# Kernel tuning notes

Hardware: AMD Instinct MI355X
Metric: run time of the kernel (lower is better)

Reference implementation:

```python
import jax, jax.numpy as jnp
import numpy as np

B, T, C = 8, 2048, 1024      # batch, timesteps, input_dim
G, E = 2, 320                # groups_dim, entries_dim
EMB = 512                    # emb_dim
D = EMB // G                 # true_emb_dim per group


def setup_inputs() -> dict:
    key = jax.random.key(0)
    k1, k2, k3 = jax.random.split(key, 3)
    X = jax.random.normal(k1, (B, T, C), dtype=jnp.float32)
    # nn.Linear(input_dim, G*E): weight (out,in) ~ N(0,1), bias zeros
    W = jax.random.normal(k2, (G * E, C), dtype=jnp.float32)
    b = jnp.zeros((G * E,), dtype=jnp.float32)
    # codebook Parameter(1, G*E, D) ~ U[0,1); stored squeezed as (G*E, D)
    codebook = jax.random.uniform(k3, (G * E, D), dtype=jnp.float32)
    return {"X": X, "W": W, "b": b, "codebook": codebook}


def reference(X, W, b, codebook):
    # Eval-mode forward of VectorQuantization (time_first=True).
    nB, nT, _ = X.shape
    logits = jnp.einsum("btc,kc->btk", X, W) + b           # (B, T, G*E)
    # Faithful to source: view (B,T,G*E) as (B*G, T*E) and argmax over last dim
    flat = logits.reshape(nB * G, nT * E)                   # (B*G, T*E)
    k = jnp.argmax(flat, axis=-1)                           # (B*G,)
    hard = jax.nn.one_hot(k, nT * E, dtype=logits.dtype)    # (B*G, T*E)
    q = hard.reshape(nB * nT, G, E)                         # (B*T, G, E)
    # (one-hot * codebook).sum over entries == per-group gather
    cb = codebook.reshape(G, E, D)                          # (G, E, D)
    out = jnp.einsum("nge,ged->ngd", q, cb)                 # (B*T, G, D)
    return out.reshape(nB, nT, G * D)                       # (B, T, emb_dim)
```

## Files before the change

kernel.cpp:

```cpp
#include <hip/hip_runtime.h>
#include <stdint.h>

#define CC    1024
#define EE    320
#define KN    640
#define DD    256
#define MTOT  16384
#define NBLK  640
#define OUT4  2097152
#define MARGIN 2.0f

typedef __attribute__((ext_vector_type(8))) short short8;
typedef __attribute__((ext_vector_type(4))) float f32x4;

__device__ __forceinline__ unsigned int f32_orderable(float x) {
    unsigned int b = __float_as_uint(x);
    return (b & 0x80000000u) ? ~b : (b | 0x80000000u);
}

__device__ __forceinline__ unsigned short bf16_rne(float x) {
    unsigned int u = __float_as_uint(x);
    return (unsigned short)((u + 0x7FFFu + ((u >> 16) & 1u)) >> 16);
}

__global__ void init_slots_kernel(unsigned long long* __restrict__ slots) {
    if (threadIdx.x < 17) slots[threadIdx.x] = 0ull;
}

__global__ __launch_bounds__(256)
void convert_kernel(const float* __restrict__ X, const float* __restrict__ W,
                    unsigned short* __restrict__ A2F, unsigned short* __restrict__ B2F,
                    unsigned long long* __restrict__ slots, float* __restrict__ out) {
    const int bid = blockIdx.x;
    const int tid = threadIdx.x;
    {
        int zidx = bid * 256 + tid;
        f32x4 z = {0.f, 0.f, 0.f, 0.f};
        if (zidx < OUT4) __builtin_nontemporal_store(z, (f32x4*)out + zidx);
    }
    const int lane = tid & 63;
    const float* src;
    unsigned short* dst;
    int unit;
    if (bid < 8192) {
        unit = (bid & 7) * 4096 + (bid >> 3) * 4 + (tid >> 6);
        src = X; dst = A2F;
    } else {
        if (bid == 8192 && tid < 17) slots[tid] = 0ull;
        unit = (bid - 8192) * 4 + (tid >> 6);
        src = W; dst = B2F;
    }
    int rt = unit >> 5, kc = unit & 31;
    int row = rt * 16 + (lane & 15);
    int col = kc * 32 + ((lane >> 4) << 3);
    const float* p = src + (size_t)row * CC + col;
    float4 v0 = *(const float4*)p;
    float4 v1 = *(const float4*)(p + 4);
    short8 hi;
    hi[0] = (short)bf16_rne(v0.x); hi[1] = (short)bf16_rne(v0.y);
    hi[2] = (short)bf16_rne(v0.z); hi[3] = (short)bf16_rne(v0.w);
    hi[4] = (short)bf16_rne(v1.x); hi[5] = (short)bf16_rne(v1.y);
    hi[6] = (short)bf16_rne(v1.z); hi[7] = (short)bf16_rne(v1.w);
    __builtin_nontemporal_store(hi, (short8*)(dst + (size_t)unit * 512 + lane * 8));
}

__global__ __launch_bounds__(256, 3)
void gemm_argmax_mfma(const unsigned short* __restrict__ A2F,
                      const unsigned short* __restrict__ B2F,
                      const float* __restrict__ X,
                      const float* __restrict__ W,
                      const float* __restrict__ bias,
                      const float* __restrict__ codebook,
                      float* __restrict__ out,
                      unsigned long long* __restrict__ slots,
                      unsigned int* __restrict__ counter) {
    __shared__ float redf[4];
    __shared__ int cnt_s;
    __shared__ int cand_s[128];
    __shared__ unsigned int done_s;
    __shared__ unsigned long long s16[16];

    const int tid  = threadIdx.x;
    const int lane = tid & 63;
    const int wave = tid >> 6;

    const int l   = blockIdx.x;
    const int xcd = l & 7;
    const int w   = l >> 3;
    const int mt  = xcd * 16 + w / 5;
    const int nt  = w % 5;
    const int m0 = mt * 128;
    const int n0 = nt * 128;

    const int wm = (wave >> 1) * 64;
    const int wn = (wave & 1) * 64;

    const unsigned short* Ap[4];
    const unsigned short* Bp[4];
#pragma unroll
    for (int t = 0; t < 4; t++) {
        Ap[t] = A2F + ((size_t)(((m0 + wm) >> 4) + t) * 32) * 512 + lane * 8;
        Bp[t] = B2F + ((size_t)(((n0 + wn) >> 4) + t) * 32) * 512 + lane * 8;
    }

    f32x4 acc[4][4] = {};
    short8 a0[4], b0[4], a1[4], b1[4];

#pragma unroll
    for (int t = 0; t < 4; t++) {
        a0[t] = *(const short8*)(Ap[t]);
        b0[t] = *(const short8*)(Bp[t]);
        Ap[t] += 512; Bp[t] += 512;
    }

#define STEP(CURA, CURB, NXTA, NXTB, IT)                                         \
    {                                                                            \
        if ((IT) < 31) {                                                         \
            _Pragma("unroll")                                                    \
            for (int t = 0; t < 4; t++) {                                        \
                NXTA[t] = *(const short8*)(Ap[t]);                               \
                NXTB[t] = *(const short8*)(Bp[t]);                               \
                Ap[t] += 512; Bp[t] += 512;                                      \
            }                                                                    \
        }                                                                        \
        _Pragma("unroll")                                                        \
        for (int ti = 0; ti < 4; ti++)                                           \
            _Pragma("unroll")                                                    \
            for (int tj = 0; tj < 4; tj++)                                       \
                acc[ti][tj] = __builtin_amdgcn_mfma_f32_16x16x32_bf16(           \
                    CURA[ti], CURB[tj], acc[ti][tj], 0, 0, 0);                   \
    }

    for (int it2 = 0; it2 < 16; it2++) {
        STEP(a0, b0, a1, b1, it2 * 2)
        STEP(a1, b1, a0, b0, it2 * 2 + 1)
    }
#undef STEP

    float bias4[4];
#pragma unroll
    for (int tj = 0; tj < 4; tj++) bias4[tj] = bias[n0 + wn + tj * 16 + (lane & 15)];

    float vmax = -3.0e38f;
#pragma unroll
    for (int ti = 0; ti < 4; ti++)
#pragma unroll
        for (int tj = 0; tj < 4; tj++)
#pragma unroll
            for (int r = 0; r < 4; r++)
                vmax = fmaxf(vmax, acc[ti][tj][r] + bias4[tj]);
#pragma unroll
    for (int off = 32; off > 0; off >>= 1)
        vmax = fmaxf(vmax, __shfl_down(vmax, off, 64));
    if (lane == 0) redf[wave] = vmax;
    if (tid == 0) cnt_s = 0;
    __syncthreads();
    float bm = fmaxf(fmaxf(redf[0], redf[1]), fmaxf(redf[2], redf[3]));
    float thresh = bm - MARGIN;

#pragma unroll
    for (int ti = 0; ti < 4; ti++) {
#pragma unroll
        for (int r = 0; r < 4; r++) {
            int m = m0 + wm + ti * 16 + (lane >> 4) * 4 + r;
#pragma unroll
            for (int tj = 0; tj < 4; tj++) {
                float v = acc[ti][tj][r] + bias4[tj];
                if (v >= thresh) {
                    int n = n0 + wn + tj * 16 + (lane & 15);
                    int idx = atomicAdd(&cnt_s, 1);
                    if (idx < 128) cand_s[idx] = (m << 10) | n;
                }
            }
        }
    }
    __syncthreads();
    int cnt = cnt_s < 128 ? cnt_s : 128;

    for (int i = 0; i < cnt; i++) {
        int mc = cand_s[i] >> 10;
        int nc = cand_s[i] & 1023;
        float4 xv = *(const float4*)(X + (size_t)mc * CC + tid * 4);
        float4 wv = *(const float4*)(W + (size_t)nc * CC + tid * 4);
        float p = xv.x * wv.x + xv.y * wv.y + xv.z * wv.z + xv.w * wv.w;
#pragma unroll
        for (int off = 32; off > 0; off >>= 1) p += __shfl_down(p, off, 64);
        if (lane == 0) redf[wave] = p;
        __syncthreads();
        if (tid == 0) {
            float tot = redf[0] + redf[1] + redf[2] + redf[3] + bias[nc];
            unsigned int c = (unsigned int)((mc & 1023) * KN + nc);
            unsigned long long pk =
                ((unsigned long long)f32_orderable(tot) << 32) |
                (unsigned long long)(~c);
            atomicMax(slots + (mc >> 10), pk);
        }
        __syncthreads();
    }

    if (tid == 0) {
        __threadfence();
        done_s = atomicAdd(counter, 1u);
    }
    __syncthreads();

    if (done_s == NBLK - 1) {
        if (tid < 16) s16[tid] = atomicAdd(slots + tid, 0ull);
        __syncthreads();
        int rr  = tid >> 4;
        int seg = tid & 15;
        unsigned long long p = s16[rr];
        unsigned int c = ~(unsigned int)(p & 0xFFFFFFFFull);
        int tl = (int)(c / KN);
        int kg = (int)(c % KN);
        int b  = rr >> 1, h = rr & 1;
        int nstar = b * 2048 + h * 1024 + tl;
        int g = kg / EE;
        const float4* src = (const float4*)(codebook + (size_t)kg * DD) + seg * 4;
        float4* dst = (float4*)(out + (size_t)nstar * 512 + (size_t)g * DD) + seg * 4;
#pragma unroll
        for (int j = 0; j < 4; j++) dst[j] = src[j];
    }
}

__global__ __launch_bounds__(256)
void zs_kernel(const unsigned long long* __restrict__ slots,
               const float* __restrict__ codebook,
               float4* __restrict__ out4) {
    int i4 = blockIdx.x * 256 + threadIdx.x;
    int n  = i4 >> 7;
    int c4 = i4 & 127;
    int b  = n >> 11;
    int h  = (n >> 10) & 1;
    unsigned long long p = slots[b * 2 + h];
    unsigned int c = ~(unsigned int)(p & 0xFFFFFFFFull);
    int tl = (int)(c / KN);
    int kg = (int)(c % KN);
    int nstar = b * 2048 + h * 1024 + tl;
    int g = kg / EE;
    float4 v = make_float4(0.f, 0.f, 0.f, 0.f);
    if (n == nstar && (c4 >> 6) == g)
        v = ((const float4*)codebook)[kg * 64 + (c4 & 63)];
    out4[i4] = v;
}

#define BM 128
#define BN 64
#define BK 32
#define LDA (BM + 4)
#define LDB (BN + 4)

__global__ __launch_bounds__(128)
void gemm_argmax_f32(const float* __restrict__ X, const float* __restrict__ W,
                     const float* __restrict__ bias,
                     unsigned long long* __restrict__ slots) {
    __shared__ float Asf[BK][LDA];
    __shared__ float Bsf[BK][LDB];
    const int tid = threadIdx.x;
    const int m0 = blockIdx.y * BM;
    const int n0 = blockIdx.x * BN;
    const int tx = tid & 7, ty = tid >> 3;
    float acc[8][8];
#pragma unroll
    for (int i = 0; i < 8; i++)
#pragma unroll
        for (int j = 0; j < 8; j++) acc[i][j] = 0.0f;
    const int lm = tid >> 3, lk = (tid & 7) * 4;
    const float* Xb = X + (size_t)m0 * CC;
    const float* Wb = W + (size_t)n0 * CC;
    for (int k0 = 0; k0 < CC; k0 += BK) {
#pragma unroll
        for (int r = 0; r < 8; r++) {
            int m = r * 16 + lm;
            float4 v = *(const float4*)(Xb + (size_t)m * CC + k0 + lk);
            Asf[lk + 0][m] = v.x; Asf[lk + 1][m] = v.y; Asf[lk + 2][m] = v.z; Asf[lk + 3][m] = v.w;
        }
#pragma unroll
        for (int r = 0; r < 4; r++) {
            int m = r * 16 + lm;
            float4 v = *(const float4*)(Wb + (size_t)m * CC + k0 + lk);
            Bsf[lk + 0][m] = v.x; Bsf[lk + 1][m] = v.y; Bsf[lk + 2][m] = v.z; Bsf[lk + 3][m] = v.w;
        }
        __syncthreads();
#pragma unroll
        for (int kk = 0; kk < BK; kk++) {
            float4 A0 = *(const float4*)&Asf[kk][ty * 8];
            float4 A1 = *(const float4*)&Asf[kk][ty * 8 + 4];
            float4 B0 = *(const float4*)&Bsf[kk][tx * 8];
            float4 B1 = *(const float4*)&Bsf[kk][tx * 8 + 4];
            float a[8] = {A0.x, A0.y, A0.z, A0.w, A1.x, A1.y, A1.z, A1.w};
            float b[8] = {B0.x, B0.y, B0.z, B0.w, B1.x, B1.y, B1.z, B1.w};
#pragma unroll
            for (int i = 0; i < 8; i++)
#pragma unroll
                for (int j = 0; j < 8; j++) acc[i][j] = fmaf(a[i], b[j], acc[i][j]);
        }
        __syncthreads();
    }
    unsigned long long best = 0ull;
#pragma unroll
    for (int i = 0; i < 8; i++) {
        int mg = m0 + ty * 8 + i;
        int tl = mg & 1023;
#pragma unroll
        for (int j = 0; j < 8; j++) {
            int kg = n0 + tx * 8 + j;
            float v = acc[i][j] + bias[kg];
            unsigned int c = (unsigned int)(tl * KN + kg);
            unsigned long long p = ((unsigned long long)f32_orderable(v) << 32) |
                                   (unsigned long long)(~c);
            if (p > best) best = p;
        }
    }
#pragma unroll
    for (int off = 32; off > 0; off >>= 1) {
        unsigned long long o = __shfl_down(best, off, 64);
        if (o > best) best = o;
    }
    __shared__ unsigned long long red2[2];
    if ((tid & 63) == 0) red2[tid >> 6] = best;
    __syncthreads();
    if (tid == 0) {
        unsigned long long b0 = red2[0], b1 = red2[1];
        atomicMax(slots + (m0 >> 10), b0 > b1 ? b0 : b1);
    }
}

extern "C" void kernel_launch(void* const* d_in, const int* in_sizes, int n_in,
                              void* d_out, int out_size, void* d_ws, size_t ws_size,
                              hipStream_t stream) {
    const float* X        = (const float*)d_in[0];
    const float* W        = (const float*)d_in[1];
    const float* bias     = (const float*)d_in[2];
    const float* codebook = (const float*)d_in[3];
    float* out = (float*)d_out;

    unsigned long long* slots = (unsigned long long*)d_ws;
    unsigned int* counter = (unsigned int*)(slots + 16);
    const size_t A_off   = 256;
    const size_t A_bytes = (size_t)MTOT * CC * 2;
    const size_t B_off   = A_off + A_bytes;
    const size_t B_bytes = (size_t)KN * CC * 2;
    const size_t need = B_off + B_bytes;

    if (ws_size >= need) {
        unsigned short* A2F = (unsigned short*)((char*)d_ws + A_off);
        unsigned short* B2F = (unsigned short*)((char*)d_ws + B_off);
        hipLaunchKernelGGL(convert_kernel, dim3(8192 + 320), dim3(256), 0, stream,
                           X, W, A2F, B2F, slots, out);
        hipLaunchKernelGGL(gemm_argmax_mfma, dim3(NBLK), dim3(256), 0, stream,
                           A2F, B2F, X, W, bias, codebook, out, slots, counter);
    } else {
        hipLaunchKernelGGL(init_slots_kernel, dim3(1), dim3(64), 0, stream, slots);
        hipLaunchKernelGGL(gemm_argmax_f32, dim3(KN / BN, MTOT / BM), dim3(128), 0, stream,
                           X, W, bias, slots);
        hipLaunchKernelGGL(zs_kernel, dim3(OUT4 / 256), dim3(256), 0, stream,
                           slots, codebook, (float4*)out);
    }
}
```

Before: 168.9 us.

## Switch argmax GEMM prefilter from bf16 to fp8 MFMA with wider margin

```diff
diff --git a/kernel.cpp b/kernel.cpp
--- a/kernel.cpp
+++ b/kernel.cpp
@@ -8,65 +8,69 @@
 #define MTOT  16384
 #define NBLK  640
 #define OUT4  2097152
-#define MARGIN 2.0f
+#define MARGIN 12.0f
 
 typedef __attribute__((ext_vector_type(8))) short short8;
 typedef __attribute__((ext_vector_type(4))) float f32x4;
+typedef __attribute__((ext_vector_type(2))) long longx2;
 
 __device__ __forceinline__ unsigned int f32_orderable(float x) {
     unsigned int b = __float_as_uint(x);
     return (b & 0x80000000u) ? ~b : (b | 0x80000000u);
 }
 
-__device__ __forceinline__ unsigned short bf16_rne(float x) {
-    unsigned int u = __float_as_uint(x);
-    return (unsigned short)((u + 0x7FFFu + ((u >> 16) & 1u)) >> 16);
-}
-
 __global__ void init_slots_kernel(unsigned long long* __restrict__ slots) {
     if (threadIdx.x < 17) slots[threadIdx.x] = 0ull;
 }
 
 __global__ __launch_bounds__(256)
 void convert_kernel(const float* __restrict__ X, const float* __restrict__ W,
-                    unsigned short* __restrict__ A2F, unsigned short* __restrict__ B2F,
+                    unsigned char* __restrict__ A2F8, unsigned char* __restrict__ B2F8,
                     unsigned long long* __restrict__ slots, float* __restrict__ out) {
     const int bid = blockIdx.x;
     const int tid = threadIdx.x;
     {
-        int zidx = bid * 256 + tid;
         f32x4 z = {0.f, 0.f, 0.f, 0.f};
-        if (zidx < OUT4) __builtin_nontemporal_store(z, (f32x4*)out + zidx);
+#pragma unroll
+        for (int j = 0; j < 2; j++) {
+            int zidx = bid * 512 + j * 256 + tid;
+            if (zidx < OUT4) __builtin_nontemporal_store(z, (f32x4*)out + zidx);
+        }
     }
     const int lane = tid & 63;
     const float* src;
-    unsigned short* dst;
-    int unit;
-    if (bid < 8192) {
-        unit = (bid & 7) * 4096 + (bid >> 3) * 4 + (tid >> 6);
-        src = X; dst = A2F;
+    unsigned char* dst;
+    int punit;
+    if (bid < 4096) {
+        punit = bid * 4 + (tid >> 6);
+        src = X; dst = A2F8;
     } else {
-        if (bid == 8192 && tid < 17) slots[tid] = 0ull;
-        unit = (bid - 8192) * 4 + (tid >> 6);
-        src = W; dst = B2F;
-    }
-    int rt = unit >> 5, kc = unit & 31;
+        if (bid == 4096 && tid < 17) slots[tid] = 0ull;
+        punit = (bid - 4096) * 4 + (tid >> 6);
+        src = W; dst = B2F8;
+    }
+    int rt = punit >> 4, kc2 = punit & 15;
     int row = rt * 16 + (lane & 15);
-    int col = kc * 32 + ((lane >> 4) << 3);
+    int col = kc2 * 64 + ((lane >> 4) << 3);
     const float* p = src + (size_t)row * CC + col;
     float4 v0 = *(const float4*)p;
     float4 v1 = *(const float4*)(p + 4);
-    short8 hi;
-    hi[0] = (short)bf16_rne(v0.x); hi[1] = (short)bf16_rne(v0.y);
-    hi[2] = (short)bf16_rne(v0.z); hi[3] = (short)bf16_rne(v0.w);
-    hi[4] = (short)bf16_rne(v1.x); hi[5] = (short)bf16_rne(v1.y);
-    hi[6] = (short)bf16_rne(v1.z); hi[7] = (short)bf16_rne(v1.w);
-    __builtin_nontemporal_store(hi, (short8*)(dst + (size_t)unit * 512 + lane * 8));
+    float4 v2 = *(const float4*)(p + 32);
+    float4 v3 = *(const float4*)(p + 36);
+    int d0 = __builtin_amdgcn_cvt_pk_fp8_f32(v0.x, v0.y, 0, false);
+    d0     = __builtin_amdgcn_cvt_pk_fp8_f32(v0.z, v0.w, d0, true);
+    int d1 = __builtin_amdgcn_cvt_pk_fp8_f32(v1.x, v1.y, 0, false);
+    d1     = __builtin_amdgcn_cvt_pk_fp8_f32(v1.z, v1.w, d1, true);
+    int d2 = __builtin_amdgcn_cvt_pk_fp8_f32(v2.x, v2.y, 0, false);
+    d2     = __builtin_amdgcn_cvt_pk_fp8_f32(v2.z, v2.w, d2, true);
+    int d3 = __builtin_amdgcn_cvt_pk_fp8_f32(v3.x, v3.y, 0, false);
+    d3     = __builtin_amdgcn_cvt_pk_fp8_f32(v3.z, v3.w, d3, true);
+    *(int4*)(dst + (size_t)punit * 1024 + lane * 16) = make_int4(d0, d1, d2, d3);
 }
 
 __global__ __launch_bounds__(256, 3)
-void gemm_argmax_mfma(const unsigned short* __restrict__ A2F,
-                      const unsigned short* __restrict__ B2F,
+void gemm_argmax_mfma(const unsigned char* __restrict__ A2F8,
+                      const unsigned char* __restrict__ B2F8,
                       const float* __restrict__ X,
                       const float* __restrict__ W,
                       const float* __restrict__ bias,
@@ -95,43 +99,45 @@
     const int wm = (wave >> 1) * 64;
     const int wn = (wave & 1) * 64;
 
-    const unsigned short* Ap[4];
-    const unsigned short* Bp[4];
+    const unsigned char* Ap[4];
+    const unsigned char* Bp[4];
 #pragma unroll
     for (int t = 0; t < 4; t++) {
-        Ap[t] = A2F + ((size_t)(((m0 + wm) >> 4) + t) * 32) * 512 + lane * 8;
-        Bp[t] = B2F + ((size_t)(((n0 + wn) >> 4) + t) * 32) * 512 + lane * 8;
+        Ap[t] = A2F8 + ((size_t)(((m0 + wm) >> 4) + t) * 16) * 1024 + lane * 16;
+        Bp[t] = B2F8 + ((size_t)(((n0 + wn) >> 4) + t) * 16) * 1024 + lane * 16;
     }
 
     f32x4 acc[4][4] = {};
-    short8 a0[4], b0[4], a1[4], b1[4];
+    longx2 a0[4], b0[4], a1[4], b1[4];
 
 #pragma unroll
     for (int t = 0; t < 4; t++) {
-        a0[t] = *(const short8*)(Ap[t]);
-        b0[t] = *(const short8*)(Bp[t]);
-        Ap[t] += 512; Bp[t] += 512;
+        a0[t] = *(const longx2*)(Ap[t]);
+        b0[t] = *(const longx2*)(Bp[t]);
+        Ap[t] += 1024; Bp[t] += 1024;
     }
 
 #define STEP(CURA, CURB, NXTA, NXTB, IT)                                         \
     {                                                                            \
-        if ((IT) < 31) {                                                         \
+        if ((IT) < 15) {                                                         \
             _Pragma("unroll")                                                    \
             for (int t = 0; t < 4; t++) {                                        \
-                NXTA[t] = *(const short8*)(Ap[t]);                               \
-                NXTB[t] = *(const short8*)(Bp[t]);                               \
-                Ap[t] += 512; Bp[t] += 512;                                      \
+                NXTA[t] = *(const longx2*)(Ap[t]);                               \
+                NXTB[t] = *(const longx2*)(Bp[t]);                               \
+                Ap[t] += 1024; Bp[t] += 1024;                                    \
             }                                                                    \
         }                                                                        \
         _Pragma("unroll")                                                        \
-        for (int ti = 0; ti < 4; ti++)                                           \
+        for (int h = 0; h < 2; h++)                                              \
             _Pragma("unroll")                                                    \
-            for (int tj = 0; tj < 4; tj++)                                       \
-                acc[ti][tj] = __builtin_amdgcn_mfma_f32_16x16x32_bf16(           \
-                    CURA[ti], CURB[tj], acc[ti][tj], 0, 0, 0);                   \
-    }
-
-    for (int it2 = 0; it2 < 16; it2++) {
+            for (int ti = 0; ti < 4; ti++)                                       \
+                _Pragma("unroll")                                                \
+                for (int tj = 0; tj < 4; tj++)                                   \
+                    acc[ti][tj] = __builtin_amdgcn_mfma_f32_16x16x32_fp8_fp8(    \
+                        CURA[ti][h], CURB[tj][h], acc[ti][tj], 0, 0, 0);         \
+    }
+
+    for (int it2 = 0; it2 < 8; it2++) {
         STEP(a0, b0, a1, b1, it2 * 2)
         STEP(a1, b1, a0, b0, it2 * 2 + 1)
     }
@@ -338,18 +344,18 @@
     unsigned long long* slots = (unsigned long long*)d_ws;
     unsigned int* counter = (unsigned int*)(slots + 16);
     const size_t A_off   = 256;
-    const size_t A_bytes = (size_t)MTOT * CC * 2;
+    const size_t A_bytes = (size_t)MTOT * CC;
     const size_t B_off   = A_off + A_bytes;
-    const size_t B_bytes = (size_t)KN * CC * 2;
+    const size_t B_bytes = (size_t)KN * CC;
     const size_t need = B_off + B_bytes;
 
     if (ws_size >= need) {
-        unsigned short* A2F = (unsigned short*)((char*)d_ws + A_off);
-        unsigned short* B2F = (unsigned short*)((char*)d_ws + B_off);
-        hipLaunchKernelGGL(convert_kernel, dim3(8192 + 320), dim3(256), 0, stream,
-                           X, W, A2F, B2F, slots, out);
+        unsigned char* A2F8 = (unsigned char*)d_ws + A_off;
+        unsigned char* B2F8 = (unsigned char*)d_ws + B_off;
+        hipLaunchKernelGGL(convert_kernel, dim3(4096 + 160), dim3(256), 0, stream,
+                           X, W, A2F8, B2F8, slots, out);
         hipLaunchKernelGGL(gemm_argmax_mfma, dim3(NBLK), dim3(256), 0, stream,
-                           A2F, B2F, X, W, bias, codebook, out, slots, counter);
+                           A2F8, B2F8, X, W, bias, codebook, out, slots, counter);
     } else {
         hipLaunchKernelGGL(init_slots_kernel, dim3(1), dim3(64), 0, stream, slots);
         hipLaunchKernelGGL(gemm_argmax_f32, dim3(KN / BN, MTOT / BM), dim3(128), 0, stream,
```

Result: faster. 153.2 us (median of 2 runs) (-9.3%).
